# Kernel optimization log

Hardware: AMD Instinct MI355X
Metric: run time of the kernel (lower is better)

Reference implementation:

```python
import jax, jax.numpy as jnp
import numpy as np

BINS = 10
T, N, D = 64, 65536, 12


def setup_inputs() -> dict:
    key = jax.random.key(0)
    ks = jax.random.split(key, 11)
    inptasksobs = jax.random.uniform(ks[0], (T, N, D), dtype=jnp.float32)
    # valid performance codes: 0 -> (0,0) zero-task, 1 -> (0,1) success, 2 -> (1,0) fail
    r = jax.random.randint(ks[1], (T, N), 0, 3)
    inptasksperf = jnp.stack([(r == 2).astype(jnp.int32), (r == 1).astype(jnp.int32)], axis=-1)
    inptaskspred = jax.random.uniform(ks[2], (N, D), dtype=jnp.float32)
    num_obs_tasks = jnp.full((N,), T, dtype=jnp.int32)
    tasksobsids = jax.random.randint(ks[3], (T, N, 1), 0, 12)
    taskspredids = jax.random.randint(ks[4], (N, 1), 0, 12)
    # capabilities live on the discretization grid (k+0.5)/BINS, as in the dataset
    disc = lambda k, shape: (jax.random.randint(k, shape, 0, BINS).astype(jnp.float32) + 0.5) / BINS
    obs_task_sens_cap_seq = disc(ks[5], (T, N))
    obs_task_proc_cap_seq = disc(ks[6], (T, N))
    pred_task_sens_cap = disc(ks[7], (N, 1))
    pred_task_proc_cap = disc(ks[8], (N, 1))
    betas = 20.0 * jax.random.uniform(ks[9], (2,), dtype=jnp.float32)
    zetas = jax.random.uniform(ks[10], (2,), dtype=jnp.float32)
    return {
        "inptasksobs": inptasksobs, "inptasksperf": inptasksperf, "inptaskspred": inptaskspred,
        "num_obs_tasks": num_obs_tasks, "tasksobsids": tasksobsids, "taskspredids": taskspredids,
        "obs_task_sens_cap_seq": obs_task_sens_cap_seq, "pred_task_sens_cap": pred_task_sens_cap,
        "obs_task_proc_cap_seq": obs_task_proc_cap_seq, "pred_task_proc_cap": pred_task_proc_cap,
        "betas": betas, "zetas": zetas,
    }


def _forward(perf, obs_sens, obs_proc, pred_sens, pred_proc, betas, zetas):
    inv = 1.0 / BINS
    n = obs_sens.shape[1]
    caps = jnp.stack([obs_sens, obs_proc], axis=-1)          # [T,N,2]
    p0 = perf[..., 0].astype(bool)                           # [T,N] fail bit
    p1 = perf[..., 1].astype(bool)                           # [T,N] success bit
    edges0 = jnp.tile(jnp.array([[0.0, 1.0]], jnp.float32), (n, 2, 1)).reshape(n, 2, 2)

    def step(edges, xs):
        cap, s0, s1 = xs                                     # cap [N,2]; s0,s1 [N]
        low, high = edges[..., 0], edges[..., 1]             # [N,2]
        succ = ((~s0) & s1)[:, None]
        fail = (s0 & (~s1))[:, None]
        # success branch: if cap > high: high = cap; elif cap > low: low = cap
        s_high = jnp.where(cap > high, cap, high)
        s_low = jnp.where((cap <= high) & (cap > low), cap, low)
        # failure branch: if cap < low: low = cap; elif cap < high: high = cap
        f_low = jnp.where(cap < low, cap, low)
        f_high = jnp.where((cap >= low) & (cap < high), cap, high)
        low2 = jnp.where(succ, s_low, jnp.where(fail, f_low, low))
        high2 = jnp.where(succ, s_high, jnp.where(fail, f_high, high))
        # degenerate-interval fixup
        eq = low2 == high2
        high3 = jnp.where(eq & (high2 == 0.0), inv, high2)
        low3 = jnp.where(eq & (high2 != 0.0), high2 - inv, low2)
        return jnp.stack([low3, high3], axis=-1), None

    edges, _ = jax.lax.scan(step, edges0, (caps, p0, p1))    # [N,2,2]
    steps = (jnp.arange(BINS, dtype=jnp.float32) + 0.5) * inv  # bin centers [10]
    low, high = edges[..., 0], edges[..., 1]                 # [N,2]
    m = ((steps >= low[..., None]) & (steps <= high[..., None])).astype(jnp.float32)  # [N,2,10]
    prob = m[:, 0, :, None] * m[:, 1, None, :]               # [N,10,10]
    prob = prob / jnp.sum(prob, axis=(1, 2), keepdims=True)
    req = jnp.concatenate([pred_sens, pred_proc], axis=-1)   # [N,2]
    # d_i(bin) = (1 + exp(beta_i * (req_i - step)))^(-zeta_i^2)
    p = betas[None, :, None] * (req[..., None] - steps)       # [N,2,10]
    d = (1.0 + jnp.exp(p)) ** (-(zetas * zetas))[None, :, None]
    trust = jnp.einsum('nj,nk,njk->n', d[:, 0], d[:, 1], prob)
    return trust[:, None]                                    # [N,1]


def reference(inptasksobs, inptasksperf, inptaskspred, num_obs_tasks, tasksobsids,
              taskspredids, obs_task_sens_cap_seq, pred_task_sens_cap,
              obs_task_proc_cap_seq, pred_task_proc_cap, betas, zetas):
    # inptasksobs / inptaskspred / num_obs_tasks / task ids are accepted but unused,
    # exactly as in the original forward (capabilityUpdate/computeTrust ignore them).
    return _forward(inptasksperf, obs_task_sens_cap_seq, obs_task_proc_cap_seq,
                    pred_task_sens_cap, pred_task_proc_cap, betas, zetas)
```

## Files before the change

kernel.cpp:

```cpp
#include <hip/hip_runtime.h>

#define NBINS 10
#define INV 0.1f
#define UNROLL 32

__device__ __forceinline__ void update_state(float& lo, float& hi, float cap,
                                             bool succ, bool fail) {
    float s_hi = (cap > hi) ? cap : hi;
    float s_lo = ((cap <= hi) && (cap > lo)) ? cap : lo;
    float f_lo = (cap < lo) ? cap : lo;
    float f_hi = ((cap >= lo) && (cap < hi)) ? cap : hi;
    float lo2 = succ ? s_lo : (fail ? f_lo : lo);
    float hi2 = succ ? s_hi : (fail ? f_hi : hi);
    bool eq = (lo2 == hi2);
    hi = (eq && (hi2 == 0.0f)) ? INV : hi2;
    lo = (eq && (hi2 != 0.0f)) ? (hi2 - INV) : lo2;
}

__global__ __launch_bounds__(256, 1) void trust_kernel(
    const long long* __restrict__ perf,
    const float* __restrict__ obs_sens,
    const float* __restrict__ obs_proc,
    const float* __restrict__ pred_sens,
    const float* __restrict__ pred_proc,
    const float* __restrict__ betas,
    const float* __restrict__ zetas,
    float*       __restrict__ out,
    int N, int T)
{
    int n = blockIdx.x * blockDim.x + threadIdx.x;
    if (n >= N) return;

    float lo0 = 0.0f, hi0 = 1.0f;
    float lo1 = 0.0f, hi1 = 1.0f;

    int t = 0;
    for (; t + UNROLL <= T; t += UNROLL) {
        long long pv[UNROLL];
        float c0[UNROLL], c1[UNROLL];
        #pragma unroll
        for (int u = 0; u < UNROLL; ++u) {
            size_t idx = (size_t)(t + u) * (size_t)N + (size_t)n;
            pv[u] = __builtin_nontemporal_load(&perf[idx]);
            c0[u] = __builtin_nontemporal_load(&obs_sens[idx]);
            c1[u] = __builtin_nontemporal_load(&obs_proc[idx]);
        }
        #pragma unroll
        for (int u = 0; u < UNROLL; ++u) {
            bool s0 = ((int)(pv[u] & 0xffffffffLL) != 0);
            bool s1 = ((int)((unsigned long long)pv[u] >> 32) != 0);
            bool succ = (!s0) && s1;
            bool fail = s0 && (!s1);
            update_state(lo0, hi0, c0[u], succ, fail);
            update_state(lo1, hi1, c1[u], succ, fail);
        }
    }
    for (; t < T; ++t) {
        size_t idx = (size_t)t * (size_t)N + (size_t)n;
        long long pv = perf[idx];
        float c0 = obs_sens[idx];
        float c1 = obs_proc[idx];
        bool s0 = ((int)(pv & 0xffffffffLL) != 0);
        bool s1 = ((int)((unsigned long long)pv >> 32) != 0);
        bool succ = (!s0) && s1;
        bool fail = s0 && (!s1);
        update_state(lo0, hi0, c0, succ, fail);
        update_state(lo1, hi1, c1, succ, fail);
    }

    float beta0 = betas[0], beta1 = betas[1];
    float z0 = zetas[0],    z1 = zetas[1];
    float e0 = -(z0 * z0),  e1 = -(z1 * z1);
    float r0 = pred_sens[n], r1 = pred_proc[n];

    float sm0 = 0.0f, sd0 = 0.0f, sm1 = 0.0f, sd1 = 0.0f;
    #pragma unroll
    for (int k = 0; k < NBINS; ++k) {
        float s = ((float)k + 0.5f) * INV;
        if (s >= lo0 && s <= hi0) {
            float p = beta0 * (r0 - s);
            sd0 += powf(1.0f + expf(p), e0);
            sm0 += 1.0f;
        }
        if (s >= lo1 && s <= hi1) {
            float p = beta1 * (r1 - s);
            sd1 += powf(1.0f + expf(p), e1);
            sm1 += 1.0f;
        }
    }

    out[n] = (sd0 / sm0) * (sd1 / sm1);
}

extern "C" void kernel_launch(void* const* d_in, const int* in_sizes, int n_in,
                              void* d_out, int out_size, void* d_ws, size_t ws_size,
                              hipStream_t stream) {
    const long long* perf   = (const long long*)d_in[1];
    const float* obs_sens   = (const float*)d_in[6];
    const float* pred_sens  = (const float*)d_in[7];
    const float* obs_proc   = (const float*)d_in[8];
    const float* pred_proc  = (const float*)d_in[9];
    const float* betas      = (const float*)d_in[10];
    const float* zetas      = (const float*)d_in[11];

    int N = in_sizes[3];
    int T = in_sizes[6] / N;

    int block = 256;
    int grid  = (N + block - 1) / block;
    trust_kernel<<<grid, block, 0, stream>>>(
        perf, obs_sens, obs_proc, pred_sens, pred_proc,
        betas, zetas, (float*)d_out, N, T);
}
```

Baseline: 301.7 us.

## Split sens/proc dimensions across half-blocks with double-buffered register prefetch

Measured after the change: 302.4 us. No clear change (+0.2%).

```diff
diff --git a/kernel.cpp b/kernel.cpp
--- a/kernel.cpp
+++ b/kernel.cpp
@@ -2,7 +2,7 @@
 
 #define NBINS 10
 #define INV 0.1f
-#define UNROLL 32
+#define U 16
 
 __device__ __forceinline__ void update_state(float& lo, float& hi, float cap,
                                              bool succ, bool fail) {
@@ -17,7 +17,31 @@
     lo = (eq && (hi2 != 0.0f)) ? (hi2 - INV) : lo2;
 }
 
-__global__ __launch_bounds__(256, 1) void trust_kernel(
+__device__ __forceinline__ void stage(long long (&pv)[U], float (&cv)[U],
+                                      const long long* __restrict__ perf,
+                                      const float* __restrict__ cap,
+                                      int t0, int N, int n)
+{
+    #pragma unroll
+    for (int u = 0; u < U; ++u) {
+        size_t idx = (size_t)(t0 + u) * (size_t)N + (size_t)n;
+        pv[u] = perf[idx];
+        cv[u] = __builtin_nontemporal_load(&cap[idx]);
+    }
+}
+
+__device__ __forceinline__ void consume(const long long (&pv)[U], const float (&cv)[U],
+                                        float& lo, float& hi)
+{
+    #pragma unroll
+    for (int u = 0; u < U; ++u) {
+        bool s0 = ((int)(pv[u] & 0xffffffffLL)) != 0;
+        bool s1 = ((int)((unsigned long long)pv[u] >> 32)) != 0;
+        update_state(lo, hi, cv[u], (!s0) && s1, s0 && (!s1));
+    }
+}
+
+__global__ __launch_bounds__(256, 2) void trust_kernel(
     const long long* __restrict__ perf,
     const float* __restrict__ obs_sens,
     const float* __restrict__ obs_proc,
@@ -28,68 +52,64 @@
     float*       __restrict__ out,
     int N, int T)
 {
-    int n = blockIdx.x * blockDim.x + threadIdx.x;
-    if (n >= N) return;
+    const int tid = threadIdx.x;
+    const int h   = tid >> 7;
+    const int ln  = tid & 127;
+    const int n   = blockIdx.x * 128 + ln;
+    const bool valid = (n < N);
+    const int nc  = valid ? n : (N - 1);
 
-    float lo0 = 0.0f, hi0 = 1.0f;
-    float lo1 = 0.0f, hi1 = 1.0f;
+    const float* __restrict__ cap = h ? obs_proc : obs_sens;
+
+    float lo = 0.0f, hi = 1.0f;
+
+    long long pA[U], pB[U];
+    float     cA[U], cB[U];
 
     int t = 0;
-    for (; t + UNROLL <= T; t += UNROLL) {
-        long long pv[UNROLL];
-        float c0[UNROLL], c1[UNROLL];
-        #pragma unroll
-        for (int u = 0; u < UNROLL; ++u) {
-            size_t idx = (size_t)(t + u) * (size_t)N + (size_t)n;
-            pv[u] = __builtin_nontemporal_load(&perf[idx]);
-            c0[u] = __builtin_nontemporal_load(&obs_sens[idx]);
-            c1[u] = __builtin_nontemporal_load(&obs_proc[idx]);
-        }
-        #pragma unroll
-        for (int u = 0; u < UNROLL; ++u) {
-            bool s0 = ((int)(pv[u] & 0xffffffffLL) != 0);
-            bool s1 = ((int)((unsigned long long)pv[u] >> 32) != 0);
-            bool succ = (!s0) && s1;
-            bool fail = s0 && (!s1);
-            update_state(lo0, hi0, c0[u], succ, fail);
-            update_state(lo1, hi1, c1[u], succ, fail);
+    const int TM = (T / (2 * U)) * (2 * U);
+    if (TM >= 2 * U) {
+        stage(pA, cA, perf, cap, 0, N, nc);
+        stage(pB, cB, perf, cap, U, N, nc);
+        while (true) {
+            consume(pA, cA, lo, hi);
+            if (t + 2 * U < TM) stage(pA, cA, perf, cap, t + 2 * U, N, nc);
+            consume(pB, cB, lo, hi);
+            if (t + 3 * U < TM) stage(pB, cB, perf, cap, t + 3 * U, N, nc);
+            t += 2 * U;
+            if (t >= TM) break;
         }
     }
     for (; t < T; ++t) {
-        size_t idx = (size_t)t * (size_t)N + (size_t)n;
+        size_t idx = (size_t)t * (size_t)N + (size_t)nc;
         long long pv = perf[idx];
-        float c0 = obs_sens[idx];
-        float c1 = obs_proc[idx];
-        bool s0 = ((int)(pv & 0xffffffffLL) != 0);
-        bool s1 = ((int)((unsigned long long)pv >> 32) != 0);
-        bool succ = (!s0) && s1;
-        bool fail = s0 && (!s1);
-        update_state(lo0, hi0, c0, succ, fail);
-        update_state(lo1, hi1, c1, succ, fail);
+        float cv = cap[idx];
+        bool s0 = ((int)(pv & 0xffffffffLL)) != 0;
+        bool s1 = ((int)((unsigned long long)pv >> 32)) != 0;
+        update_state(lo, hi, cv, (!s0) && s1, s0 && (!s1));
     }
 
-    float beta0 = betas[0], beta1 = betas[1];
-    float z0 = zetas[0],    z1 = zetas[1];
-    float e0 = -(z0 * z0),  e1 = -(z1 * z1);
-    float r0 = pred_sens[n], r1 = pred_proc[n];
+    float beta = betas[h];
+    float z    = zetas[h];
+    float e    = -(z * z);
+    float r    = h ? pred_proc[nc] : pred_sens[nc];
 
-    float sm0 = 0.0f, sd0 = 0.0f, sm1 = 0.0f, sd1 = 0.0f;
+    float sm = 0.0f, sd = 0.0f;
     #pragma unroll
     for (int k = 0; k < NBINS; ++k) {
         float s = ((float)k + 0.5f) * INV;
-        if (s >= lo0 && s <= hi0) {
-            float p = beta0 * (r0 - s);
-            sd0 += powf(1.0f + expf(p), e0);
-            sm0 += 1.0f;
-        }
-        if (s >= lo1 && s <= hi1) {
-            float p = beta1 * (r1 - s);
-            sd1 += powf(1.0f + expf(p), e1);
-            sm1 += 1.0f;
+        if (s >= lo && s <= hi) {
+            float p = beta * (r - s);
+            sd += powf(1.0f + expf(p), e);
+            sm += 1.0f;
         }
     }
+    float v = sd / sm;
 
-    out[n] = (sd0 / sm0) * (sd1 / sm1);
+    __shared__ float red[128];
+    if (h) red[ln] = v;
+    __syncthreads();
+    if (!h && valid) out[n] = v * red[ln];
 }
 
 extern "C" void kernel_launch(void* const* d_in, const int* in_sizes, int n_in,
@@ -107,7 +127,7 @@
     int T = in_sizes[6] / N;
 
     int block = 256;
-    int grid  = (N + block - 1) / block;
+    int grid  = (N + 127) / 128;
     trust_kernel<<<grid, block, 0, stream>>>(
         perf, obs_sens, obs_proc, pred_sens, pred_proc,
         betas, zetas, (float*)d_out, N, T);
```
